# Kernel tuning notes

Measured on AMD Instinct MI355X. Metric: run time of the kernel, lower is better.

Reference implementation:

```python
import jax, jax.numpy as jnp
import numpy as np

B_SZ, T, C_DIM, N = 16, 2048, 128, 64
STEP = 0.01
LN_EPS = 1e-5


def _cplx(re, im):
    return (re + 1j * im).astype(jnp.complex64)


def s4_kernel(L_real, L_imag, P_real, P_imag, B_real, B_imag, C_real, C_imag, L):
    """DPLR generating-function kernel (annotated-S4 kernel_DPLR), vectorized over channels.
    Returns real kernel of shape (L, C)."""
    Lam = _cplx(jnp.minimum(L_real, 1e-4), L_imag)          # (C, N)
    P = _cplx(P_real, P_imag)                                # (C, N)
    Bm = _cplx(B_real, B_imag)                               # (C, N)
    Cm = _cplx(C_real, C_imag)                               # (C, N)
    Omega = jnp.exp(-2j * jnp.pi * jnp.arange(L) / L).astype(jnp.complex64)  # (L,)
    g = (2.0 / STEP) * ((1.0 - Omega) / (1.0 + Omega))       # (L,)
    c2 = 2.0 / (1.0 + Omega)                                 # (L,)

    def cauchy(v):  # v: (C, N) -> (L, C)
        return (v[None, :, :] / (g[:, None, None] - Lam[None, :, :])).sum(-1)

    k00 = cauchy(jnp.conj(Cm) * Bm)
    k01 = cauchy(jnp.conj(Cm) * P)
    k10 = cauchy(jnp.conj(P) * Bm)
    k11 = cauchy(jnp.conj(P) * P)
    at_roots = c2[:, None] * (k00 - k01 * (1.0 / (1.0 + k11)) * k10)  # (L, C)
    return jnp.fft.ifft(at_roots, n=L, axis=0).real          # (L, C)


def setup_inputs() -> dict:
    key = jax.random.key(0)
    ks = jax.random.split(key, 12)
    s = 1.0 / np.sqrt(N)
    return {
        "x": jax.random.normal(ks[0], (B_SZ, T, C_DIM), jnp.float32),
        "ln_gamma": jnp.ones((C_DIM,), jnp.float32),
        "ln_beta": jnp.zeros((C_DIM,), jnp.float32),
        "L_real": -0.5 * jnp.abs(jax.random.normal(ks[1], (C_DIM, N), jnp.float32)),
        "L_imag": jax.random.normal(ks[2], (C_DIM, N), jnp.float32) * float(np.pi),
        "P_real": jax.random.normal(ks[3], (C_DIM, N), jnp.float32) * s,
        "P_imag": jax.random.normal(ks[4], (C_DIM, N), jnp.float32) * s,
        "B_real": jax.random.normal(ks[5], (C_DIM, N), jnp.float32) * s,
        "B_imag": jax.random.normal(ks[6], (C_DIM, N), jnp.float32) * s,
        "C_real": jax.random.normal(ks[7], (C_DIM, N), jnp.float32) * float(np.sqrt(0.5)),
        "C_imag": jax.random.normal(ks[8], (C_DIM, N), jnp.float32) * float(np.sqrt(0.5)),
        "D": jnp.ones((C_DIM,), jnp.float32),
        "W_out": jax.random.normal(ks[9], (C_DIM, C_DIM), jnp.float32) / float(np.sqrt(C_DIM)),
        "b_out": jnp.zeros((C_DIM,), jnp.float32),
    }


def reference(x, ln_gamma, ln_beta, L_real, L_imag, P_real, P_imag,
              B_real, B_imag, C_real, C_imag, D, W_out, b_out):
    # pre-LayerNorm over channels
    mu = x.mean(-1, keepdims=True)
    var = ((x - mu) ** 2).mean(-1, keepdims=True)
    y = (x - mu) / jnp.sqrt(var + LN_EPS) * ln_gamma + ln_beta   # (B, T, C)

    # S4 FFT convolution (training path)
    kernel = s4_kernel(L_real, L_imag, P_real, P_imag,
                       B_real, B_imag, C_real, C_imag, T)       # (T, C)
    kf = jnp.fft.rfft(kernel, n=2 * T, axis=0)                  # (T+1, C)
    uf = jnp.fft.rfft(y, n=2 * T, axis=1)                        # (B, T+1, C)
    conv = jnp.fft.irfft(uf * kf[None], n=2 * T, axis=1)[:, :T, :]
    ssm_out = conv + D * y                                       # skip D*u

    # GELU (exact) -> Linear -> residual
    h = jax.nn.gelu(ssm_out, approximate=False)
    out = jnp.einsum("btc,oc->bto", h, W_out) + b_out
    return out + x
```

## Files before the change

### kernel.cpp

```cpp
#include <hip/hip_runtime.h>


#define PAD(i) ((i) + ((i) >> 4))

using bf16x8 = __attribute__((ext_vector_type(8))) short;
using f32x4 = __attribute__((ext_vector_type(4))) float;
typedef unsigned short ushort_t;

static __device__ __forceinline__ float2 cmulf(float2 a, float2 b) {
  return make_float2(a.x * b.x - a.y * b.y, a.x * b.y + a.y * b.x);
}
static __device__ __forceinline__ float2 cadd(float2 a, float2 b) { return make_float2(a.x + b.x, a.y + b.y); }
static __device__ __forceinline__ float2 csub(float2 a, float2 b) { return make_float2(a.x - b.x, a.y - b.y); }
static __device__ __forceinline__ float2 cconj(float2 a) { return make_float2(a.x, -a.y); }
static __device__ __forceinline__ float gelu1(float x) { return 0.5f * x * (1.0f + erff(x * 0.70710678f)); }
static __device__ __forceinline__ ushort_t f2bf(float f) {
  unsigned int u = __float_as_uint(f);
  u += 0x7FFFu + ((u >> 16) & 1u);
  return (ushort_t)(u >> 16);
}
static __device__ __forceinline__ float bf2f(ushort_t u) {
  return __uint_as_float(((unsigned int)u) << 16);
}
static __device__ __forceinline__ float2 twf(float rev) {
  return make_float2(__builtin_amdgcn_cosf(rev), -__builtin_amdgcn_sinf(rev));
}
static __device__ __forceinline__ float2 twi(float rev) {
  return make_float2(__builtin_amdgcn_cosf(rev), __builtin_amdgcn_sinf(rev));
}

template <bool INV>
static __device__ __forceinline__ void bf4g(float2& a, float2& b, float2& c, float2& d, float2 w1) {
  float2 t0 = cadd(a, c), t1 = csub(a, c), t2 = cadd(b, d), t3 = csub(b, d);
  float2 w2 = cmulf(w1, w1), w3 = cmulf(w2, w1);
  float2 o0 = cadd(t0, t2);
  float2 o1 = cmulf(csub(t0, t2), w2);
  float2 o2, o3;
  if (!INV) {
    o2 = cmulf(make_float2(t1.x + t3.y, t1.y - t3.x), w1);
    o3 = cmulf(make_float2(t1.x - t3.y, t1.y + t3.x), w3);
  } else {
    o2 = cmulf(make_float2(t1.x - t3.y, t1.y + t3.x), w1);
    o3 = cmulf(make_float2(t1.x + t3.y, t1.y - t3.x), w3);
  }
  a = o0; b = o1; c = o2; d = o3;
}
static __device__ __forceinline__ void bf4f(float2& a, float2& b, float2& c, float2& d, float2 w1) {
  bf4g<false>(a, b, c, d, w1);
}
static __device__ __forceinline__ void bf4f1(float2& a, float2& b, float2& c, float2& d) {
  float2 t0 = cadd(a, c), t1 = csub(a, c), t2 = cadd(b, d), t3 = csub(b, d);
  a = cadd(t0, t2);
  b = csub(t0, t2);
  c = make_float2(t1.x + t3.y, t1.y - t3.x);
  d = make_float2(t1.x - t3.y, t1.y + t3.x);
}
static __device__ __forceinline__ void bf4f_z(float2 a, float2 b, float2 w1,
                                              float2& o0, float2& o1, float2& o2, float2& o3) {
  float2 w2 = cmulf(w1, w1), w3 = cmulf(w2, w1);
  o0 = cadd(a, b);
  o1 = cmulf(csub(a, b), w2);
  o2 = cmulf(make_float2(a.x + b.y, a.y - b.x), w1);
  o3 = cmulf(make_float2(a.x - b.y, a.y + b.x), w3);
}
template <bool INV>
static __device__ __forceinline__ void bf4h(float2& a, float2& b, float2& c, float2& d, float2 u1) {
  float2 u2 = cmulf(u1, u1);
  float2 tb = cmulf(b, u2), td = cmulf(d, u2);
  float2 a1 = cadd(a, tb), b1 = csub(a, tb), c1 = cadd(c, td), d1 = csub(c, td);
  float2 tc = cmulf(c1, u1), te = cmulf(d1, u1);
  a = cadd(a1, tc);
  c = csub(a1, tc);
  if (INV) {
    b = make_float2(b1.x - te.y, b1.y + te.x);
    d = make_float2(b1.x + te.y, b1.y - te.x);
  } else {
    b = make_float2(b1.x + te.y, b1.y - te.x);
    d = make_float2(b1.x - te.y, b1.y + te.x);
  }
}
static __device__ __forceinline__ void bf4i(float2& a, float2& b, float2& c, float2& d, float2 u1) {
  bf4h<true>(a, b, c, d, u1);
}
static __device__ __forceinline__ void bf4i1(float2& a, float2& b, float2& c, float2& d) {
  float2 a1 = cadd(a, b), b1 = csub(a, b), c1 = cadd(c, d), d1 = csub(c, d);
  a = cadd(a1, c1);
  c = csub(a1, c1);
  b = make_float2(b1.x - d1.y, b1.y + d1.x);
  d = make_float2(b1.x + d1.y, b1.y - d1.x);
}

#define W256R 0.9238795325112867f
#define W256I -0.3826834323650898f
#define W512R 0.7071067811865476f
#define W512I -0.7071067811865476f
#define W768R 0.3826834323650898f
#define W768I -0.9238795325112867f

__global__ __launch_bounds__(256) void k_ln_ar(
    const float* __restrict__ x, const float* __restrict__ gamma, const float* __restrict__ beta,
    ushort_t* __restrict__ y_bf,
    const float* __restrict__ Lr, const float* __restrict__ Li,
    const float* __restrict__ Pr, const float* __restrict__ Pi,
    const float* __restrict__ Br, const float* __restrict__ Bi,
    const float* __restrict__ Cr, const float* __restrict__ Ci,
    float2* __restrict__ arr) {
  __shared__ __align__(16) char sm[17536];
  const int tid = threadIdx.x;
  if (blockIdx.x < 1024) {
    float* tile = (float*)sm;
    float* sg = (float*)(sm + 16512);
    float* sb = (float*)(sm + 17024);
    const int b = blockIdx.x >> 6;
    const int t0 = (blockIdx.x & 63) << 5;
    if (tid < 128) { sg[tid] = gamma[tid]; sb[tid] = beta[tid]; }
    const float4* __restrict__ xb4 = (const float4*)(x + ((size_t)b * 2048 + t0) * 128);
#pragma unroll
    for (int r = 0; r < 4; ++r) {
      int idx = tid + 256 * r;
      int t = idx >> 5, j = idx & 31;
      float4 v4 = xb4[idx];
      float* dst = &tile[t * 129 + 4 * j];
      dst[0] = v4.x; dst[1] = v4.y; dst[2] = v4.z; dst[3] = v4.w;
    }
    __syncthreads();
    const int row = tid >> 3, sgp = tid & 7;
    float sum = 0.f, sq = 0.f;
#pragma unroll
    for (int i = 0; i < 16; ++i) {
      float v = tile[row * 129 + sgp * 16 + i];
      sum += v;
      sq += v * v;
    }
    sum += __shfl_xor(sum, 1); sq += __shfl_xor(sq, 1);
    sum += __shfl_xor(sum, 2); sq += __shfl_xor(sq, 2);
    sum += __shfl_xor(sum, 4); sq += __shfl_xor(sq, 4);
    float mean = sum * (1.0f / 128.0f);
    float var = sq * (1.0f / 128.0f) - mean * mean;
    float rstd = 1.0f / sqrtf(var + 1e-5f);
#pragma unroll
    for (int i = 0; i < 16; ++i) {
      int cc = sgp * 16 + i;
      float v = tile[row * 129 + cc];
      tile[row * 129 + cc] = (v - mean) * rstd * sg[cc] + sb[cc];
    }
    __syncthreads();
    ushort_t* __restrict__ yb = y_bf + (size_t)b * 128 * 2048 + t0;
#pragma unroll
    for (int r = 0; r < 4; ++r) {
      int idx = tid + 256 * r;
      int cc = idx >> 3, tl4 = (idx & 7) * 4;
      ushort4 o4;
      o4.x = f2bf(tile[(tl4 + 0) * 129 + cc]);
      o4.y = f2bf(tile[(tl4 + 1) * 129 + cc]);
      o4.z = f2bf(tile[(tl4 + 2) * 129 + cc]);
      o4.w = f2bf(tile[(tl4 + 3) * 129 + cc]);
      *(ushort4*)(yb + (size_t)cc * 2048 + tl4) = o4;
    }
  } else {
    float2* sLam = (float2*)sm;
    float2* sv00 = sLam + 64;
    float2* sv01 = sLam + 128;
    float2* sv10 = sLam + 192;
    float2* sv11 = sLam + 256;
    const int id = blockIdx.x - 1024;
    const int c = id >> 3;
    const int l = ((id & 7) << 8) + tid;
    if (tid < 64) {
      int i = c * 64 + tid;
      float lr = fminf(Lr[i], 1e-4f), li = Li[i];
      float pr = Pr[i], pi = Pi[i];
      float br = Br[i], bi = Bi[i];
      float cr = Cr[i], ci = Ci[i];
      sLam[tid] = make_float2(lr, li);
      sv00[tid] = make_float2(cr * br + ci * bi, cr * bi - ci * br);
      sv01[tid] = make_float2(cr * pr + ci * pi, cr * pi - ci * pr);
      sv10[tid] = make_float2(pr * br + pi * bi, pr * bi - pi * br);
      sv11[tid] = make_float2(pr * pr + pi * pi, 0.0f);
    }
    __syncthreads();
    float theta = (-6.2831855f * (float)l) * (1.0f / 2048.0f);
    float om_i, om_r;
    sincosf(theta, &om_i, &om_r);
    float pr_ = 1.0f + om_r, pi_ = om_i;
    float mr_ = 1.0f - om_r, mi_ = -om_i;
    float invd = __builtin_amdgcn_rcpf(fmaf(pr_, pr_, pi_ * pi_));
    float gr = 200.0f * ((mr_ * pr_ + mi_ * pi_) * invd);
    float gi = 200.0f * ((mi_ * pr_ - mr_ * pi_) * invd);
    float c2r = 2.0f * pr_ * invd, c2i = -2.0f * pi_ * invd;
    float s00r = 0.f, s00i = 0.f, s01r = 0.f, s01i = 0.f;
    float s10r = 0.f, s10i = 0.f, s11r = 0.f, s11i = 0.f;
#pragma unroll 8
    for (int n = 0; n < 64; ++n) {
      float2 lam = sLam[n];
      float dr = gr - lam.x, di = gi - lam.y;
      float idn = __builtin_amdgcn_rcpf(fmaf(dr, dr, di * di));
      float ir = dr * idn, ii = -di * idn;
      float2 v;
      v = sv00[n]; s00r += v.x * ir - v.y * ii; s00i += v.x * ii + v.y * ir;
      v = sv01[n]; s01r += v.x * ir - v.y * ii; s01i += v.x * ii + v.y * ir;
      v = sv10[n]; s10r += v.x * ir - v.y * ii; s10i += v.x * ii + v.y * ir;
      v = sv11[n]; s11r += v.x * ir - v.y * ii; s11i += v.x * ii + v.y * ir;
    }
    float dr2 = 1.0f + s11r, di2 = s11i;
    float idn2 = __builtin_amdgcn_rcpf(fmaf(dr2, dr2, di2 * di2));
    float rr = dr2 * idn2, ri = -di2 * idn2;
    float t1r = s01r * rr - s01i * ri, t1i = s01r * ri + s01i * rr;
    float t2r = t1r * s10r - t1i * s10i, t2i = t1r * s10i + t1i * s10r;
    float fr = s00r - t2r, fi = s00i - t2i;
    arr[(size_t)c * 2048 + l] = make_float2(c2r * fr - c2i * fi, c2r * fi + c2i * fr);
  }
}

template <int Q, bool INV>
static __device__ __forceinline__ void kfs_dif(float2* s, int tid) {
  constexpr float SCR = (float)(2048 / (4 * Q)) * (1.0f / 2048.0f);
  int k = tid;
  int j = k & (Q - 1);
  int i = ((k - j) << 2) + j;
  float2 w1 = INV ? twi((float)j * SCR) : twf((float)j * SCR);
  float2 a = s[PAD(i)], b = s[PAD(i + Q)], c2 = s[PAD(i + 2 * Q)], d = s[PAD(i + 3 * Q)];
  bf4g<INV>(a, b, c2, d, w1);
  s[PAD(i)] = a; s[PAD(i + Q)] = b; s[PAD(i + 2 * Q)] = c2; s[PAD(i + 3 * Q)] = d;
  __syncthreads();
}
template <int Q>
static __device__ __forceinline__ void kfs_dit(float2* s, int tid) {
  constexpr float SCR = (float)(2048 / (4 * Q)) * (1.0f / 2048.0f);
  int k = tid;
  int j = k & (Q - 1);
  int i = ((k - j) << 2) + j;
  float2 u1 = twf((float)j * SCR);
  float2 a = s[PAD(i)], b = s[PAD(i + Q)], c2 = s[PAD(i + 2 * Q)], d = s[PAD(i + 3 * Q)];
  bf4h<false>(a, b, c2, d, u1);
  s[PAD(i)] = a; s[PAD(i + Q)] = b; s[PAD(i + 2 * Q)] = c2; s[PAD(i + 3 * Q)] = d;
  __syncthreads();
}
static __device__ __forceinline__ void kfs_r2(float2* s, int tid) {
#pragma unroll
  for (int m = 0; m < 2; ++m) {
    int k = tid + 512 * m;
    int i = 2 * k;
    float2 a = s[PAD(i)], b = s[PAD(i + 1)];
    s[PAD(i)] = cadd(a, b);
    s[PAD(i + 1)] = csub(a, b);
  }
  __syncthreads();
}

__global__ __launch_bounds__(512) void k_kf(const float2* __restrict__ arr, float2* __restrict__ kf) {
  __shared__ float2 s[2176];
  const int tid = threadIdx.x;
  const int c = blockIdx.x;
  const float2* __restrict__ ac = arr + (size_t)c * 2048;
  float2* __restrict__ kfc = kf + (size_t)c * 4096;
#pragma unroll
  for (int m = 0; m < 4; ++m) {
    int q = tid + 512 * m;
    float2 aq = ac[q];
    s[PAD(q)] = aq;
    float2 am = ac[(2048 - q) & 2047];
    kfc[__brev((unsigned)q) >> 21] =
        make_float2((aq.x + am.x) * (0.5f / 4096.0f), (aq.y - am.y) * (0.5f / 4096.0f));
  }
  __syncthreads();
  kfs_dif<512, true>(s, tid);
  kfs_dif<128, true>(s, tid);
  kfs_dif<32, true>(s, tid);
  kfs_dif<8, true>(s, tid);
  kfs_dif<2, true>(s, tid);
  kfs_r2(s, tid);
#pragma unroll
  for (int m = 0; m < 4; ++m) {
    int p = tid + 512 * m;
    int t = (int)(__brev((unsigned)p) >> 21);
    float2 w = twf((float)t * (1.0f / 4096.0f));
    float kr = s[PAD(p)].x * (1.0f / 8388608.0f);
    s[PAD(p)] = make_float2(kr * w.x, kr * w.y);
  }
  __syncthreads();
  kfs_r2(s, tid);
  kfs_dit<2>(s, tid);
  kfs_dit<8>(s, tid);
  kfs_dit<32>(s, tid);
  kfs_dit<128>(s, tid);
  kfs_dit<512>(s, tid);
#pragma unroll
  for (int m = 0; m < 4; ++m) {
    int q = tid + 512 * m;
    kfc[2048 + (int)(__brev((unsigned)q) >> 21)] = s[PAD(q)];
  }
}

__global__ __launch_bounds__(256) void k_conv(const ushort_t* __restrict__ y_bf,
                                              const float2* __restrict__ kf,
                                              const float* __restrict__ D,
                                              ushort_t* __restrict__ h_bf) {
  __shared__ float2 s[4352];
  const int tid = threadIdx.x;
  const int p = blockIdx.x;
  const int b = p >> 7, c = p & 127;
  const ushort_t* __restrict__ r1 = y_bf + (size_t)(b * 128 + c) * 2048;
  const ushort_t* __restrict__ r2 = y_bf + (size_t)((b + 8) * 128 + c) * 2048;
  ushort_t* __restrict__ hb1 = h_bf + (size_t)(b * 128 + c) * 2048;
  ushort_t* __restrict__ hb2 = h_bf + (size_t)((b + 8) * 128 + c) * 2048;

  const float2 K1 = make_float2(W256R, W256I);
  const float2 K2 = make_float2(W512R, W512I);
  const float2 K3 = make_float2(W768R, W768I);

  float2 v[16];
  {
    float2 ya[8];
#pragma unroll
    for (int e = 0; e < 8; ++e)
      ya[e] = make_float2(bf2f(r1[tid + 256 * e]), bf2f(r2[tid + 256 * e]));
    const float2 wt = twf((float)tid * (1.0f / 4096.0f));
    bf4f_z(ya[0], ya[4], wt,            v[0], v[4], v[8], v[12]);
    bf4f_z(ya[1], ya[5], cmulf(wt, K1), v[1], v[5], v[9], v[13]);
    bf4f_z(ya[2], ya[6], cmulf(wt, K2), v[2], v[6], v[10], v[14]);
    bf4f_z(ya[3], ya[7], cmulf(wt, K3), v[3], v[7], v[11], v[15]);
  }
  {
    const float2 wq = twf((float)tid * (1.0f / 1024.0f));
    bf4f(v[0], v[1], v[2], v[3], wq);
    bf4f(v[4], v[5], v[6], v[7], wq);
    bf4f(v[8], v[9], v[10], v[11], wq);
    bf4f(v[12], v[13], v[14], v[15], wq);
  }
  {
    const int wb0 = tid + (tid >> 4);
#pragma unroll
    for (int e = 0; e < 16; ++e) s[272 * e + wb0] = v[e];
  }
  __syncthreads();
  const int a_ = tid >> 4, b_ = tid & 15;
  const int rbB = 272 * a_ + b_;
#pragma unroll
  for (int e = 0; e < 16; ++e) v[e] = s[rbB + 17 * e];
  {
    const float2 wb = twf((float)b_ * (1.0f / 256.0f));
    bf4f(v[0], v[4], v[8], v[12], wb);
    bf4f(v[1], v[5], v[9], v[13], cmulf(wb, K1));
    bf4f(v[2], v[6], v[10], v[14], cmulf(wb, K2));
    bf4f(v[3], v[7], v[11], v[15], cmulf(wb, K3));
  }
  {
    const float2 w16 = twf((float)b_ * (1.0f / 64.0f));
    bf4f(v[0], v[1], v[2], v[3], w16);
    bf4f(v[4], v[5], v[6], v[7], w16);
    bf4f(v[8], v[9], v[10], v[11], w16);
    bf4f(v[12], v[13], v[14], v[15], w16);
  }
#pragma unroll
  for (int e = 0; e < 16; ++e) s[rbB + 17 * e] = v[e];
  __syncthreads();
#pragma unroll
  for (int e = 0; e < 16; ++e) v[e] = s[17 * tid + e];
  bf4f1(v[0], v[4], v[8], v[12]);
  bf4f(v[1], v[5], v[9], v[13], K1);
  bf4f(v[2], v[6], v[10], v[14], K2);
  bf4f(v[3], v[7], v[11], v[15], K3);
  bf4f1(v[0], v[1], v[2], v[3]);
  bf4f1(v[4], v[5], v[6], v[7]);
  bf4f1(v[8], v[9], v[10], v[11]);
  bf4f1(v[12], v[13], v[14], v[15]);
  {
    const float dsc = D[c] * (1.0f / 4096.0f);
    const float2* __restrict__ kfc = kf + (size_t)c * 4096 + 16 * tid;
#pragma unroll
    for (int e = 0; e < 16; ++e) {
      float2 kv = kfc[e];
      kv.x += dsc;
      v[e] = cmulf(v[e], kv);
    }
  }
  bf4i1(v[0], v[1], v[2], v[3]);
  bf4i1(v[4], v[5], v[6], v[7]);
  bf4i1(v[8], v[9], v[10], v[11]);
  bf4i1(v[12], v[13], v[14], v[15]);
  bf4i1(v[0], v[4], v[8], v[12]);
  bf4i(v[1], v[5], v[9], v[13], cconj(K1));
  bf4i(v[2], v[6], v[10], v[14], cconj(K2));
  bf4i(v[3], v[7], v[11], v[15], cconj(K3));
#pragma unroll
  for (int e = 0; e < 16; ++e) s[17 * tid + e] = v[e];
  __syncthreads();
#pragma unroll
  for (int e = 0; e < 16; ++e) v[e] = s[rbB + 17 * e];
  {
    const float2 w16c = twi((float)b_ * (1.0f / 64.0f));
    bf4i(v[0], v[1], v[2], v[3], w16c);
    bf4i(v[4], v[5], v[6], v[7], w16c);
    bf4i(v[8], v[9], v[10], v[11], w16c);
    bf4i(v[12], v[13], v[14], v[15], w16c);
  }
  {
    const float2 wbc = twi((float)b_ * (1.0f / 256.0f));
    bf4i(v[0], v[4], v[8], v[12], wbc);
    bf4i(v[1], v[5], v[9], v[13], cmulf(wbc, cconj(K1)));
    bf4i(v[2], v[6], v[10], v[14], cmulf(wbc, cconj(K2)));
    bf4i(v[3], v[7], v[11], v[15], cmulf(wbc, cconj(K3)));
  }
#pragma unroll
  for (int e = 0; e < 16; ++e) s[rbB + 17 * e] = v[e];
  __syncthreads();
  {
    const int wb0 = tid + (tid >> 4);
#pragma unroll
    for (int e = 0; e < 16; ++e) v[e] = s[272 * e + wb0];
  }
  {
    const float2 wqc = twi((float)tid * (1.0f / 1024.0f));
    bf4i(v[0], v[1], v[2], v[3], wqc);
    bf4i(v[4], v[5], v[6], v[7], wqc);
    bf4i(v[8], v[9], v[10], v[11], wqc);
    bf4i(v[12], v[13], v[14], v[15], wqc);
  }
  const float2 wtc = twi((float)tid * (1.0f / 4096.0f));
  auto fin = [&](float2 va, float2 vb, float2 vc2, float2 vd, float2 u1, int e0) {
    float2 u2 = cmulf(u1, u1);
    float2 tb = cmulf(vb, u2), td = cmulf(vd, u2);
    float2 a1 = cadd(va, tb), b1 = csub(va, tb), c1 = cadd(vc2, td), d1 = csub(vc2, td);
    float2 tc = cmulf(c1, u1), te = cmulf(d1, u1);
    float2 oa = cadd(a1, tc);
    float2 ob = make_float2(b1.x - te.y, b1.y + te.x);
    int i0 = tid + 256 * e0;
    hb1[i0] = f2bf(gelu1(oa.x));
    hb2[i0] = f2bf(gelu1(oa.y));
    hb1[i0 + 1024] = f2bf(gelu1(ob.x));
    hb2[i0 + 1024] = f2bf(gelu1(ob.y));
  };
  fin(v[0], v[4], v[8], v[12], wtc, 0);
  fin(v[1], v[5], v[9], v[13], cmulf(wtc, cconj(K1)), 1);
  fin(v[2], v[6], v[10], v[14], cmulf(wtc, cconj(K2)), 2);
  fin(v[3], v[7], v[11], v[15], cmulf(wtc, cconj(K3)), 3);
}

__global__ __launch_bounds__(256) void k_out(const ushort_t* __restrict__ h_bf,
                                             const float* __restrict__ W,
                                             const float* __restrict__ bout,
                                             const float* __restrict__ x,
                                             float* __restrict__ out) {
  __shared__ __align__(16) char smem[52224];
  ushort_t* Wl = (ushort_t*)smem;
  ushort_t* hl = (ushort_t*)(smem + 34816);
  const int tid = threadIdx.x;
  const int b = blockIdx.x >> 5;
  const int t0 = (blockIdx.x & 31) << 6;

  {
    const float4* __restrict__ W4 = (const float4*)W;
#pragma unroll
    for (int r = 0; r < 16; ++r) {
      int idx = tid + 256 * r;
      int o = idx >> 5, j = idx & 31;
      float4 w4 = W4[o * 32 + j];
      int sc = (((j >> 1) ^ (o & 15)) << 3) + 4 * (j & 1);
      ushort4 u;
      u.x = f2bf(w4.x); u.y = f2bf(w4.y); u.z = f2bf(w4.z); u.w = f2bf(w4.w);
      *(ushort4*)&Wl[o * 136 + sc] = u;
    }
  }
  {
#pragma unroll
    for (int r = 0; r < 8; ++r) {
      int idx = tid + 256 * r;
      int cc = idx >> 4, t4 = (idx & 15) * 4;
      ushort4 hv = *(const ushort4*)&h_bf[((size_t)(b * 128 + cc)) * 2048 + t0 + t4];
      int cb = cc >> 3, clo = cc & 7;
#pragma unroll
      for (int i = 0; i < 4; ++i) {
        int t = t4 + i;
        hl[t * 136 + (((cb ^ (t & 15)) << 3) + clo)] = ((const ushort_t*)&hv)[i];
      }
    }
  }
  __syncthreads();

  const int l = tid & 63;
  const int w = tid >> 6;
  const int tl = l & 15;
  const int g = l >> 4;
  f32x4 acc[8];
#pragma unroll
  for (int i = 0; i < 8; ++i) acc[i] = (f32x4){0.f, 0.f, 0.f, 0.f};

#pragma unroll
  for (int ks = 0; ks < 4; ++ks) {
    int cb = ks * 4 + g;
    int col = ((cb ^ tl) << 3);
    bf16x8 bfrag = *(const bf16x8*)&hl[(16 * w + tl) * 136 + col];
#pragma unroll
    for (int ot = 0; ot < 8; ++ot) {
      bf16x8 afrag = *(const bf16x8*)&Wl[(ot * 16 + tl) * 136 + col];
      acc[ot] = __builtin_amdgcn_mfma_f32_16x16x32_bf16(afrag, bfrag, acc[ot], 0, 0, 0);
    }
  }
  const int t = t0 + 16 * w + tl;
  const size_t rowoff = ((size_t)b * 2048 + t) * 128;
#pragma unroll
  for (int ot = 0; ot < 8; ++ot) {
    int o = ot * 16 + g * 4;
    float4 xv = *(const float4*)&x[rowoff + o];
    float4 bo4 = *(const float4*)&bout[o];
    float4 v;
    v.x = acc[ot][0] + bo4.x + xv.x;
    v.y = acc[ot][1] + bo4.y + xv.y;
    v.z = acc[ot][2] + bo4.z + xv.z;
    v.w = acc[ot][3] + bo4.w + xv.w;
    *(float4*)&out[rowoff + o] = v;
  }
}


extern "C" void kernel_launch(void* const* d_in, const int* in_sizes, int n_in,
                              void* d_out, int out_size, void* d_ws, size_t ws_size,
                              hipStream_t stream) {
  (void)in_sizes; (void)n_in; (void)out_size; (void)ws_size;
  const float* x  = (const float*)d_in[0];
  const float* g  = (const float*)d_in[1];
  const float* be = (const float*)d_in[2];
  const float* Lr = (const float*)d_in[3];
  const float* Li = (const float*)d_in[4];
  const float* Pr = (const float*)d_in[5];
  const float* Pi = (const float*)d_in[6];
  const float* Br = (const float*)d_in[7];
  const float* Bi = (const float*)d_in[8];
  const float* Cr = (const float*)d_in[9];
  const float* Ci = (const float*)d_in[10];
  const float* D  = (const float*)d_in[11];
  const float* W  = (const float*)d_in[12];
  const float* bo = (const float*)d_in[13];
  float* out = (float*)d_out;

  char* ws = (char*)d_ws;
  ushort_t* y_bf = (ushort_t*)ws;
  float2*   arr  = (float2*)(ws + (16u << 20));
  float2*   kfb  = (float2*)(ws + (18u << 20));
  ushort_t* h_bf = (ushort_t*)(ws + (22u << 20));

  hipLaunchKernelGGL(k_ln_ar, dim3(2048), dim3(256), 0, stream,
                     x, g, be, y_bf, Lr, Li, Pr, Pi, Br, Bi, Cr, Ci, arr);
  hipLaunchKernelGGL(k_kf,   dim3(128),  dim3(512), 0, stream, arr, kfb);
  hipLaunchKernelGGL(k_conv, dim3(1024), dim3(256), 0, stream, y_bf, kfb, D, h_bf);
  hipLaunchKernelGGL(k_out,  dim3(512),  dim3(256), 0, stream, h_bf, W, bo, x, out);
}
```

Before: 70.44 us.

## Fuse DPLR at-roots evaluation and kernel FFT into the LayerNorm kernel

The separate k_kf launch is merged into the LayerNorm/at-roots kernel. Each of 128 channel blocks (512 threads) now evaluates all 2048 at-roots values into shared memory and runs the kernel FFT in place, so the global `arr` round trip and one kernel launch disappear. The LayerNorm blocks are also widened to 512 threads covering 64 timesteps each. The trade-off is that the at-roots Cauchy sums move from 1024 parallel blocks to 128 blocks that each loop four times serially, which lengthens those blocks' critical path.

Measured after the change: 81.75 us. 1.16x slower.

```diff
diff --git a/kernel.cpp b/kernel.cpp
--- a/kernel.cpp
+++ b/kernel.cpp
@@ -97,27 +97,63 @@
 #define W768R 0.3826834323650898f
 #define W768I -0.9238795325112867f
 
-__global__ __launch_bounds__(256) void k_ln_ar(
+template <int Q, bool INV>
+static __device__ __forceinline__ void kfs_dif(float2* s, int tid) {
+  constexpr float SCR = (float)(2048 / (4 * Q)) * (1.0f / 2048.0f);
+  int k = tid;
+  int j = k & (Q - 1);
+  int i = ((k - j) << 2) + j;
+  float2 w1 = INV ? twi((float)j * SCR) : twf((float)j * SCR);
+  float2 a = s[PAD(i)], b = s[PAD(i + Q)], c2 = s[PAD(i + 2 * Q)], d = s[PAD(i + 3 * Q)];
+  bf4g<INV>(a, b, c2, d, w1);
+  s[PAD(i)] = a; s[PAD(i + Q)] = b; s[PAD(i + 2 * Q)] = c2; s[PAD(i + 3 * Q)] = d;
+  __syncthreads();
+}
+template <int Q>
+static __device__ __forceinline__ void kfs_dit(float2* s, int tid) {
+  constexpr float SCR = (float)(2048 / (4 * Q)) * (1.0f / 2048.0f);
+  int k = tid;
+  int j = k & (Q - 1);
+  int i = ((k - j) << 2) + j;
+  float2 u1 = twf((float)j * SCR);
+  float2 a = s[PAD(i)], b = s[PAD(i + Q)], c2 = s[PAD(i + 2 * Q)], d = s[PAD(i + 3 * Q)];
+  bf4h<false>(a, b, c2, d, u1);
+  s[PAD(i)] = a; s[PAD(i + Q)] = b; s[PAD(i + 2 * Q)] = c2; s[PAD(i + 3 * Q)] = d;
+  __syncthreads();
+}
+static __device__ __forceinline__ void kfs_r2(float2* s, int tid) {
+#pragma unroll
+  for (int m = 0; m < 2; ++m) {
+    int k = tid + 512 * m;
+    int i = 2 * k;
+    float2 a = s[PAD(i)], b = s[PAD(i + 1)];
+    s[PAD(i)] = cadd(a, b);
+    s[PAD(i + 1)] = csub(a, b);
+  }
+  __syncthreads();
+}
+
+__global__ __launch_bounds__(512) void k_ln_arkf(
     const float* __restrict__ x, const float* __restrict__ gamma, const float* __restrict__ beta,
     ushort_t* __restrict__ y_bf,
     const float* __restrict__ Lr, const float* __restrict__ Li,
     const float* __restrict__ Pr, const float* __restrict__ Pi,
     const float* __restrict__ Br, const float* __restrict__ Bi,
     const float* __restrict__ Cr, const float* __restrict__ Ci,
-    float2* __restrict__ arr) {
-  __shared__ __align__(16) char sm[17536];
+    float2* __restrict__ kfb) {
+  __shared__ __align__(16) char sm[34304];
   const int tid = threadIdx.x;
-  if (blockIdx.x < 1024) {
+  if (blockIdx.x < 512) {
     float* tile = (float*)sm;
-    float* sg = (float*)(sm + 16512);
-    float* sb = (float*)(sm + 17024);
-    const int b = blockIdx.x >> 6;
-    const int t0 = (blockIdx.x & 63) << 5;
+    float* sg = (float*)(sm + 33024);
+    float* sb = (float*)(sm + 33536);
+    const int b = blockIdx.x >> 5;
+    const int t0 = (blockIdx.x & 31) << 6;
     if (tid < 128) { sg[tid] = gamma[tid]; sb[tid] = beta[tid]; }
     const float4* __restrict__ xb4 = (const float4*)(x + ((size_t)b * 2048 + t0) * 128);
 #pragma unroll
     for (int r = 0; r < 4; ++r) {
-      int idx = tid + 256 * r;
+      int idx = tid + 512 * r;
       int t = idx >> 5, j = idx & 31;
       float4 v4 = xb4[idx];
       float* dst = &tile[t * 129 + 4 * j];
@@ -148,8 +184,8 @@
     ushort_t* __restrict__ yb = y_bf + (size_t)b * 128 * 2048 + t0;
 #pragma unroll
     for (int r = 0; r < 4; ++r) {
-      int idx = tid + 256 * r;
-      int cc = idx >> 3, tl4 = (idx & 7) * 4;
+      int idx = tid + 512 * r;
+      int cc = idx >> 4, tl4 = (idx & 15) * 4;
       ushort4 o4;
       o4.x = f2bf(tile[(tl4 + 0) * 129 + cc]);
       o4.y = f2bf(tile[(tl4 + 1) * 129 + cc]);
@@ -158,14 +194,13 @@
       *(ushort4*)(yb + (size_t)cc * 2048 + tl4) = o4;
     }
   } else {
-    float2* sLam = (float2*)sm;
+    float2* s = (float2*)sm;
+    float2* sLam = (float2*)(sm + 17408);
     float2* sv00 = sLam + 64;
     float2* sv01 = sLam + 128;
     float2* sv10 = sLam + 192;
     float2* sv11 = sLam + 256;
-    const int id = blockIdx.x - 1024;
-    const int c = id >> 3;
-    const int l = ((id & 7) << 8) + tid;
+    const int c = blockIdx.x - 512;
     if (tid < 64) {
       int i = c * 64 + tid;
       float lr = fminf(Lr[i], 1e-4f), li = Li[i];
@@ -179,116 +214,77 @@
       sv11[tid] = make_float2(pr * pr + pi * pi, 0.0f);
     }
     __syncthreads();
-    float theta = (-6.2831855f * (float)l) * (1.0f / 2048.0f);
-    float om_i, om_r;
-    sincosf(theta, &om_i, &om_r);
-    float pr_ = 1.0f + om_r, pi_ = om_i;
-    float mr_ = 1.0f - om_r, mi_ = -om_i;
-    float invd = __builtin_amdgcn_rcpf(fmaf(pr_, pr_, pi_ * pi_));
-    float gr = 200.0f * ((mr_ * pr_ + mi_ * pi_) * invd);
-    float gi = 200.0f * ((mi_ * pr_ - mr_ * pi_) * invd);
-    float c2r = 2.0f * pr_ * invd, c2i = -2.0f * pi_ * invd;
-    float s00r = 0.f, s00i = 0.f, s01r = 0.f, s01i = 0.f;
-    float s10r = 0.f, s10i = 0.f, s11r = 0.f, s11i = 0.f;
+#pragma unroll 1
+    for (int m = 0; m < 4; ++m) {
+      int l = tid + 512 * m;
+      float theta = (-6.2831855f * (float)l) * (1.0f / 2048.0f);
+      float om_i, om_r;
+      sincosf(theta, &om_i, &om_r);
+      float pr_ = 1.0f + om_r, pi_ = om_i;
+      float mr_ = 1.0f - om_r, mi_ = -om_i;
+      float invd = __builtin_amdgcn_rcpf(fmaf(pr_, pr_, pi_ * pi_));
+      float gr = 200.0f * ((mr_ * pr_ + mi_ * pi_) * invd);
+      float gi = 200.0f * ((mi_ * pr_ - mr_ * pi_) * invd);
+      float c2r = 2.0f * pr_ * invd, c2i = -2.0f * pi_ * invd;
+      float s00r = 0.f, s00i = 0.f, s01r = 0.f, s01i = 0.f;
+      float s10r = 0.f, s10i = 0.f, s11r = 0.f, s11i = 0.f;
 #pragma unroll 8
-    for (int n = 0; n < 64; ++n) {
-      float2 lam = sLam[n];
-      float dr = gr - lam.x, di = gi - lam.y;
-      float idn = __builtin_amdgcn_rcpf(fmaf(dr, dr, di * di));
-      float ir = dr * idn, ii = -di * idn;
-      float2 v;
-      v = sv00[n]; s00r += v.x * ir - v.y * ii; s00i += v.x * ii + v.y * ir;
-      v = sv01[n]; s01r += v.x * ir - v.y * ii; s01i += v.x * ii + v.y * ir;
-      v = sv10[n]; s10r += v.x * ir - v.y * ii; s10i += v.x * ii + v.y * ir;
-      v = sv11[n]; s11r += v.x * ir - v.y * ii; s11i += v.x * ii + v.y * ir;
-    }
-    float dr2 = 1.0f + s11r, di2 = s11i;
-    float idn2 = __builtin_amdgcn_rcpf(fmaf(dr2, dr2, di2 * di2));
-    float rr = dr2 * idn2, ri = -di2 * idn2;
-    float t1r = s01r * rr - s01i * ri, t1i = s01r * ri + s01i * rr;
-    float t2r = t1r * s10r - t1i * s10i, t2i = t1r * s10i + t1i * s10r;
-    float fr = s00r - t2r, fi = s00i - t2i;
-    arr[(size_t)c * 2048 + l] = make_float2(c2r * fr - c2i * fi, c2r * fi + c2i * fr);
-  }
-}
-
-template <int Q, bool INV>
-static __device__ __forceinline__ void kfs_dif(float2* s, int tid) {
-  constexpr float SCR = (float)(2048 / (4 * Q)) * (1.0f / 2048.0f);
-  int k = tid;
-  int j = k & (Q - 1);
-  int i = ((k - j) << 2) + j;
-  float2 w1 = INV ? twi((float)j * SCR) : twf((float)j * SCR);
-  float2 a = s[PAD(i)], b = s[PAD(i + Q)], c2 = s[PAD(i + 2 * Q)], d = s[PAD(i + 3 * Q)];
-  bf4g<INV>(a, b, c2, d, w1);
-  s[PAD(i)] = a; s[PAD(i + Q)] = b; s[PAD(i + 2 * Q)] = c2; s[PAD(i + 3 * Q)] = d;
-  __syncthreads();
-}
-template <int Q>
-static __device__ __forceinline__ void kfs_dit(float2* s, int tid) {
-  constexpr float SCR = (float)(2048 / (4 * Q)) * (1.0f / 2048.0f);
-  int k = tid;
-  int j = k & (Q - 1);
-  int i = ((k - j) << 2) + j;
-  float2 u1 = twf((float)j * SCR);
-  float2 a = s[PAD(i)], b = s[PAD(i + Q)], c2 = s[PAD(i + 2 * Q)], d = s[PAD(i + 3 * Q)];
-  bf4h<false>(a, b, c2, d, u1);
-  s[PAD(i)] = a; s[PAD(i + Q)] = b; s[PAD(i + 2 * Q)] = c2; s[PAD(i + 3 * Q)] = d;
-  __syncthreads();
-}
-static __device__ __forceinline__ void kfs_r2(float2* s, int tid) {
-#pragma unroll
-  for (int m = 0; m < 2; ++m) {
-    int k = tid + 512 * m;
-    int i = 2 * k;
-    float2 a = s[PAD(i)], b = s[PAD(i + 1)];
-    s[PAD(i)] = cadd(a, b);
-    s[PAD(i + 1)] = csub(a, b);
-  }
-  __syncthreads();
-}
-
-__global__ __launch_bounds__(512) void k_kf(const float2* __restrict__ arr, float2* __restrict__ kf) {
-  __shared__ float2 s[2176];
-  const int tid = threadIdx.x;
-  const int c = blockIdx.x;
-  const float2* __restrict__ ac = arr + (size_t)c * 2048;
-  float2* __restrict__ kfc = kf + (size_t)c * 4096;
-#pragma unroll
-  for (int m = 0; m < 4; ++m) {
-    int q = tid + 512 * m;
-    float2 aq = ac[q];
-    s[PAD(q)] = aq;
-    float2 am = ac[(2048 - q) & 2047];
-    kfc[__brev((unsigned)q) >> 21] =
-        make_float2((aq.x + am.x) * (0.5f / 4096.0f), (aq.y - am.y) * (0.5f / 4096.0f));
-  }
-  __syncthreads();
-  kfs_dif<512, true>(s, tid);
-  kfs_dif<128, true>(s, tid);
-  kfs_dif<32, true>(s, tid);
-  kfs_dif<8, true>(s, tid);
-  kfs_dif<2, true>(s, tid);
-  kfs_r2(s, tid);
-#pragma unroll
-  for (int m = 0; m < 4; ++m) {
-    int p = tid + 512 * m;
-    int t = (int)(__brev((unsigned)p) >> 21);
-    float2 w = twf((float)t * (1.0f / 4096.0f));
-    float kr = s[PAD(p)].x * (1.0f / 8388608.0f);
-    s[PAD(p)] = make_float2(kr * w.x, kr * w.y);
-  }
-  __syncthreads();
-  kfs_r2(s, tid);
-  kfs_dit<2>(s, tid);
-  kfs_dit<8>(s, tid);
-  kfs_dit<32>(s, tid);
-  kfs_dit<128>(s, tid);
-  kfs_dit<512>(s, tid);
-#pragma unroll
-  for (int m = 0; m < 4; ++m) {
-    int q = tid + 512 * m;
-    kfc[2048 + (int)(__brev((unsigned)q) >> 21)] = s[PAD(q)];
+      for (int n = 0; n < 64; ++n) {
+        float2 lam = sLam[n];
+        float dr = gr - lam.x, di = gi - lam.y;
+        float idn = __builtin_amdgcn_rcpf(fmaf(dr, dr, di * di));
+        float ir = dr * idn, ii = -di * idn;
+        float2 v;
+        v = sv00[n]; s00r += v.x * ir - v.y * ii; s00i += v.x * ii + v.y * ir;
+        v = sv01[n]; s01r += v.x * ir - v.y * ii; s01i += v.x * ii + v.y * ir;
+        v = sv10[n]; s10r += v.x * ir - v.y * ii; s10i += v.x * ii + v.y * ir;
+        v = sv11[n]; s11r += v.x * ir - v.y * ii; s11i += v.x * ii + v.y * ir;
+      }
+      float dr2 = 1.0f + s11r, di2 = s11i;
+      float idn2 = __builtin_amdgcn_rcpf(fmaf(dr2, dr2, di2 * di2));
+      float rr = dr2 * idn2, ri = -di2 * idn2;
+      float t1r = s01r * rr - s01i * ri, t1i = s01r * ri + s01i * rr;
+      float t2r = t1r * s10r - t1i * s10i, t2i = t1r * s10i + t1i * s10r;
+      float fr = s00r - t2r, fi = s00i - t2i;
+      s[PAD(l)] = make_float2(c2r * fr - c2i * fi, c2r * fi + c2i * fr);
+    }
+    __syncthreads();
+    float2* __restrict__ kfc = kfb + (size_t)c * 4096;
+#pragma unroll
+    for (int m = 0; m < 4; ++m) {
+      int q = tid + 512 * m;
+      float2 aq = s[PAD(q)];
+      float2 am = s[PAD((2048 - q) & 2047)];
+      kfc[__brev((unsigned)q) >> 21] =
+          make_float2((aq.x + am.x) * (0.5f / 4096.0f), (aq.y - am.y) * (0.5f / 4096.0f));
+    }
+    __syncthreads();
+    kfs_dif<512, true>(s, tid);
+    kfs_dif<128, true>(s, tid);
+    kfs_dif<32, true>(s, tid);
+    kfs_dif<8, true>(s, tid);
+    kfs_dif<2, true>(s, tid);
+    kfs_r2(s, tid);
+#pragma unroll
+    for (int m = 0; m < 4; ++m) {
+      int p = tid + 512 * m;
+      int t = (int)(__brev((unsigned)p) >> 21);
+      float2 w = twf((float)t * (1.0f / 4096.0f));
+      float kr = s[PAD(p)].x * (1.0f / 8388608.0f);
+      s[PAD(p)] = make_float2(kr * w.x, kr * w.y);
+    }
+    __syncthreads();
+    kfs_r2(s, tid);
+    kfs_dit<2>(s, tid);
+    kfs_dit<8>(s, tid);
+    kfs_dit<32>(s, tid);
+    kfs_dit<128>(s, tid);
+    kfs_dit<512>(s, tid);
+#pragma unroll
+    for (int m = 0; m < 4; ++m) {
+      int q = tid + 512 * m;
+      kfc[2048 + (int)(__brev((unsigned)q) >> 21)] = s[PAD(q)];
+    }
   }
 }
 
@@ -536,13 +532,11 @@
 
   char* ws = (char*)d_ws;
   ushort_t* y_bf = (ushort_t*)ws;
-  float2*   arr  = (float2*)(ws + (16u << 20));
   float2*   kfb  = (float2*)(ws + (18u << 20));
   ushort_t* h_bf = (ushort_t*)(ws + (22u << 20));
 
-  hipLaunchKernelGGL(k_ln_ar, dim3(2048), dim3(256), 0, stream,
-                     x, g, be, y_bf, Lr, Li, Pr, Pi, Br, Bi, Cr, Ci, arr);
-  hipLaunchKernelGGL(k_kf,   dim3(128),  dim3(512), 0, stream, arr, kfb);
+  hipLaunchKernelGGL(k_ln_arkf, dim3(640), dim3(512), 0, stream,
+                     x, g, be, y_bf, Lr, Li, Pr, Pi, Br, Bi, Cr, Ci, kfb);
   hipLaunchKernelGGL(k_conv, dim3(1024), dim3(256), 0, stream, y_bf, kfb, D, h_bf);
   hipLaunchKernelGGL(k_out,  dim3(512),  dim3(256), 0, stream, h_bf, W, bo, x, out);
 }
```
